# Optimization experiments

Hardware: AMD Instinct MI355X
Metric: run time of the kernel (lower is better)

## Reference

```python
import jax, jax.numpy as jnp
import numpy as np

B, S, H, NH, NF = 128, 1024, 768, 8, 8
FUSED = 3 * H + NF  # 2312


def _lin(k, o, i):
    return jax.random.normal(k, (o, i), jnp.float32) * (1.0 / np.sqrt(i))


def setup_inputs() -> dict:
    key = jax.random.key(0)
    ks = jax.random.split(key, 20)
    last_hidden = jax.random.normal(ks[0], (B, S, H), jnp.float32)
    arousal_feats = jax.random.normal(ks[1], (B, NF), jnp.float32)
    sep1 = jax.random.randint(ks[2], (B,), 2, 800)
    sep2 = jnp.minimum(sep1 + jax.random.randint(ks[3], (B,), 2, 200), S - 1)
    return {
        "last_hidden": last_hidden,
        "arousal_feats": arousal_feats,
        "sep1": sep1,
        "sep2": sep2,
        "in_proj_w": _lin(ks[4], 3 * H, H),
        "in_proj_b": jnp.zeros((3 * H,), jnp.float32),
        "out_w": _lin(ks[5], H, H),
        "out_b": jnp.zeros((H,), jnp.float32),
        "ln_g": jnp.ones((NF,), jnp.float32),
        "ln_b": jnp.zeros((NF,), jnp.float32),
        "va_w1": _lin(ks[6], 512, FUSED),
        "va_b1": jnp.zeros((512,), jnp.float32),
        "va_w2": _lin(ks[7], 128, 512),
        "va_b2": jnp.zeros((128,), jnp.float32),
        "va_w3": _lin(ks[8], 2, 128),
        "va_b3": jnp.zeros((2,), jnp.float32),
        "pol_w": _lin(ks[9], 3, FUSED),
        "pol_b": jnp.zeros((3,), jnp.float32),
        "aro_w": _lin(ks[10], 3, FUSED),
        "aro_b": jnp.zeros((3,), jnp.float32),
    }


def reference(last_hidden, arousal_feats, sep1, sep2, in_proj_w, in_proj_b,
              out_w, out_b, ln_g, ln_b, va_w1, va_b1, va_w2, va_b2,
              va_w3, va_b3, pol_w, pol_b, aro_w, aro_b):
    b, s, h = last_hidden.shape
    nh, dh = NH, h // NH
    pos = jnp.arange(s)[None, :]  # [1,S]
    # ragged boundaries -> masks (honors s1>1 / s2>s1+1 fallbacks to CLS token)
    text_mask = jnp.where((sep1 > 1)[:, None], (pos >= 1) & (pos < sep1[:, None]), pos == 0)
    asp_mask = jnp.where((sep2 > sep1 + 1)[:, None], (pos > sep1[:, None]) & (pos < sep2[:, None]), pos == 0)
    amf = asp_mask.astype(last_hidden.dtype)
    asp_query = (last_hidden * amf[..., None]).sum(1) / amf.sum(1)[:, None]  # [B,H]
    # MultiheadAttention with a single query per sample, keys/values masked to text span
    wq, wk, wv = jnp.split(in_proj_w, 3, axis=0)
    bq, bk, bv = jnp.split(in_proj_b, 3)
    q = (asp_query @ wq.T + bq).reshape(b, nh, dh)
    k = (last_hidden @ wk.T + bk).reshape(b, s, nh, dh)
    v = (last_hidden @ wv.T + bv).reshape(b, s, nh, dh)
    scale = 1.0 / np.sqrt(dh)
    scores = jnp.einsum('bhd,bshd->bhs', q, k) * scale
    scores = jnp.where(text_mask[:, None, :], scores, -jnp.inf)
    attn = jax.nn.softmax(scores, axis=-1)
    ctx = jnp.einsum('bhs,bshd->bhd', attn, v).reshape(b, h)
    cross = ctx @ out_w.T + out_b  # [B,H]
    # ArousalFeatureNorm ~ LayerNorm over feature dim
    mu = arousal_feats.mean(-1, keepdims=True)
    var = arousal_feats.var(-1, keepdims=True)
    aro_n = (arousal_feats - mu) / jnp.sqrt(var + 1e-5) * ln_g + ln_b
    fused = jnp.concatenate([last_hidden[:, 0], cross, asp_query, aro_n], axis=-1)
    hdn = jax.nn.gelu(fused @ va_w1.T + va_b1, approximate=False)
    hdn = jax.nn.gelu(hdn @ va_w2.T + va_b2, approximate=False)
    va = hdn @ va_w3.T + va_b3
    pol = fused @ pol_w.T + pol_b
    aro = fused @ aro_w.T + aro_b
    return (va, pol, aro)
```

## Files before the change

### kernel.cpp

```cpp
#include <hip/hip_runtime.h>
#include <hip/hip_bf16.h>
#include <math.h>

#define B 128
#define S 1024
#define H 768
#define NH 8
#define DH 96
#define FUSED 2312
#define FPAD 2432
#define KSPLIT 19
#define KCHUNK 128
#define ASL 8
#define NSL 8
#define FCH 16
#define SCALE 0.10206207261596575f
#define GELU_C 0.70710678118654752f

__device__ __forceinline__ float dot4(float4 a, float4 b) {
    return a.x * b.x + a.y * b.y + a.z * b.z + a.w * b.w;
}

__global__ void aspq_part_kernel(const float* __restrict__ lh,
                                 const int* __restrict__ sep1,
                                 const int* __restrict__ sep2,
                                 float* __restrict__ aspp) {
    int b = blockIdx.x, z = blockIdx.y, t = threadIdx.x;
    int s1 = sep1[b], s2 = sep2[b];
    int lo, hi;
    if (s2 > s1 + 1) { lo = s1 + 1; hi = s2; } else { lo = 0; hi = 1; }
    const float* base = lh + ((size_t)b * S) * H + 4 * t;
    float4 a = {0.f, 0.f, 0.f, 0.f};
    for (int s = lo + z; s < hi; s += ASL) {
        float4 r = *(const float4*)(base + (size_t)s * H);
        a.x += r.x; a.y += r.y; a.z += r.z; a.w += r.w;
    }
    *(float4*)(aspp + (size_t)z * (B * H) + b * H + 4 * t) = a;
}

__global__ void qu_kernel(const float* __restrict__ aspp,
                          const int* __restrict__ sep1,
                          const int* __restrict__ sep2,
                          const float* __restrict__ wq,
                          const float* __restrict__ bq,
                          const float* __restrict__ wk,
                          float* __restrict__ aspq,
                          float* __restrict__ U) {
    int b = blockIdx.x, h = blockIdx.y, t = threadIdx.x;
    int s1 = sep1[b], s2 = sep2[b];
    int lo, hi;
    if (s2 > s1 + 1) { lo = s1 + 1; hi = s2; } else { lo = 0; hi = 1; }
    float inv = 1.0f / (float)(hi - lo);
    __shared__ float aq[H];
    __shared__ float qh[DH];
    for (int c = t; c < H; c += 256) {
        float a = 0.f;
#pragma unroll
        for (int z = 0; z < ASL; ++z)
            a += aspp[(size_t)z * (B * H) + b * H + c];
        a *= inv;
        aq[c] = a;
        if (h == 0) aspq[b * H + c] = a;
    }
    __syncthreads();
    int wave = t >> 6, lane = t & 63;
#pragma unroll
    for (int i = 0; i < 24; ++i) {
        int d = wave * 24 + i;
        const float* wrow = wq + (size_t)(h * DH + d) * H;
        float a = 0.f;
#pragma unroll
        for (int j = 0; j < H / 64; ++j) a += wrow[lane + 64 * j] * aq[lane + 64 * j];
        for (int off = 32; off; off >>= 1) a += __shfl_xor(a, off);
        if (lane == 0) qh[d] = a + bq[h * DH + d];
    }
    __syncthreads();
    float u0 = 0.f, u1 = 0.f, u2 = 0.f;
    for (int d = 0; d < DH; ++d) {
        const float* wrow = wk + (size_t)(h * DH + d) * H;
        float qd = qh[d];
        u0 += qd * wrow[t];
        u1 += qd * wrow[t + 256];
        u2 += qd * wrow[t + 512];
    }
    float* Ub = U + ((size_t)b * NH + h) * H;
    Ub[t] = u0; Ub[t + 256] = u1; Ub[t + 512] = u2;
}

__global__ __launch_bounds__(512) void flash_kernel(
        const float* __restrict__ lhg,
        const float* __restrict__ U,
        const int* __restrict__ sep1,
        float* __restrict__ Op,
        float* __restrict__ mlb) {
    int b = blockIdx.x, z = blockIdx.y, t = threadIdx.x;
    int wave = t >> 6, lane = t & 63;
    int s1 = sep1[b];
    int tlo = (s1 > 1) ? 1 : 0;
    int thi = (s1 > 1) ? s1 : 1;
    int span = thi - tlo;
    int nrows = (span > z) ? ((span - z - 1) / NSL + 1) : 0;

    __shared__ float lhs[FCH][H];

    const float4* Uh = (const float4*)(U + ((size_t)b * NH + wave) * H);
    float4 u0 = Uh[lane], u1 = Uh[lane + 64], u2 = Uh[lane + 128];
    float4 O0 = {0.f, 0.f, 0.f, 0.f}, O1 = O0, O2 = O0;
    float m = -1e30f, l = 0.f;

    int rid = t >> 5;
    int cid = t & 31;

    for (int j0 = 0; j0 < nrows; j0 += FCH) {
        int nv = min(FCH, nrows - j0);
        if (rid < nv) {
            int sg = tlo + z + NSL * (j0 + rid);
            const float4* row = (const float4*)(lhg + ((size_t)b * S + sg) * H);
            float4* dst = (float4*)lhs[rid];
#pragma unroll
            for (int k = 0; k < 6; ++k) dst[cid + 32 * k] = row[cid + 32 * k];
        }
        __syncthreads();
        for (int r = 0; r < nv; ++r) {
            const float4* xr = (const float4*)lhs[r];
            float4 x0 = xr[lane], x1 = xr[lane + 64], x2 = xr[lane + 128];
            float s = dot4(u0, x0) + dot4(u1, x1) + dot4(u2, x2);
            for (int off = 32; off; off >>= 1) s += __shfl_xor(s, off);
            s *= SCALE;
            if (s <= m) {
                float p = __expf(s - m);
                l += p;
                O0.x += p * x0.x; O0.y += p * x0.y; O0.z += p * x0.z; O0.w += p * x0.w;
                O1.x += p * x1.x; O1.y += p * x1.y; O1.z += p * x1.z; O1.w += p * x1.w;
                O2.x += p * x2.x; O2.y += p * x2.y; O2.z += p * x2.z; O2.w += p * x2.w;
            } else {
                float c = __expf(m - s);
                m = s;
                l = l * c + 1.0f;
                O0.x = O0.x * c + x0.x; O0.y = O0.y * c + x0.y;
                O0.z = O0.z * c + x0.z; O0.w = O0.w * c + x0.w;
                O1.x = O1.x * c + x1.x; O1.y = O1.y * c + x1.y;
                O1.z = O1.z * c + x1.z; O1.w = O1.w * c + x1.w;
                O2.x = O2.x * c + x2.x; O2.y = O2.y * c + x2.y;
                O2.z = O2.z * c + x2.z; O2.w = O2.w * c + x2.w;
            }
        }
        __syncthreads();
    }
    float4* Ob = (float4*)(Op + (((size_t)z * B + b) * NH + wave) * H);
    Ob[lane] = O0; Ob[lane + 64] = O1; Ob[lane + 128] = O2;
    if (lane == 0) {
        float* ml = mlb + ((size_t)z * B + b) * NH * 2;
        ml[2 * wave]     = m;
        ml[2 * wave + 1] = l;
    }
}

__global__ void mergectx_kernel(const float* __restrict__ Op,
                                const float* __restrict__ mlb,
                                const float* __restrict__ wv,
                                const float* __restrict__ bv,
                                float* __restrict__ ctx) {
    int b = blockIdx.x, h = blockIdx.y, t = threadIdx.x;
    float M = -1e30f;
#pragma unroll
    for (int z = 0; z < NSL; ++z)
        M = fmaxf(M, mlb[(((size_t)z * B + b) * NH + h) * 2]);
    float wz[NSL], L = 0.f;
#pragma unroll
    for (int z = 0; z < NSL; ++z) {
        const float* ml = mlb + (((size_t)z * B + b) * NH + h) * 2;
        float e = __expf(ml[0] - M);
        wz[z] = e;
        L += e * ml[1];
    }
    float Li = 1.0f / L;
    __shared__ float wsum[H];
    for (int c = t; c < H; c += 256) {
        float a = 0.f;
#pragma unroll
        for (int z = 0; z < NSL; ++z)
            a += wz[z] * Op[(((size_t)z * B + b) * NH + h) * H + c];
        wsum[c] = a * Li;
    }
    __syncthreads();
    int wave = t >> 6, lane = t & 63;
#pragma unroll
    for (int i = 0; i < 24; ++i) {
        int d = wave * 24 + i;
        const float* wrow = wv + (size_t)(h * DH + d) * H;
        float a = 0.f;
#pragma unroll
        for (int j = 0; j < H / 64; ++j) a += wrow[lane + 64 * j] * wsum[lane + 64 * j];
        for (int off = 32; off; off >>= 1) a += __shfl_xor(a, off);
        if (lane == 0) ctx[b * H + h * DH + d] = a + bv[h * DH + d];
    }
}

template <int TAG, bool KCL>
__global__ void gemm_kernel(const float* __restrict__ A, int lda, int a_bs,
                            const float* __restrict__ W, int ldw, int w_bs,
                            float* __restrict__ C, int ldc, int c_bs,
                            int M, int N, int K, int kclamp) {
    A += (size_t)blockIdx.z * a_bs;
    W += (size_t)blockIdx.z * w_bs;
    C += (size_t)blockIdx.z * c_bs;
    int kcl = KCL ? (kclamp - (int)blockIdx.z * w_bs) : 0;
    int n0 = blockIdx.x * 32, m0 = blockIdx.y * 32;
    __shared__ float As[32][33];
    __shared__ float Ws[32][33];
    int t = threadIdx.x;
    int tx = t & 31, ty = t >> 5;
    int lr = t >> 3, lc = (t & 7) * 4;
    float acc[4] = {0.f, 0.f, 0.f, 0.f};
    for (int k0 = 0; k0 < K; k0 += 32) {
        {
            float4 a = *(const float4*)(A + (size_t)(m0 + lr) * lda + k0 + lc);
            As[lr][lc] = a.x; As[lr][lc + 1] = a.y;
            As[lr][lc + 2] = a.z; As[lr][lc + 3] = a.w;
        }
        {
            int kk = k0 + lc;
            if (KCL) kk = min(kk, kcl);
            float4 w = *(const float4*)(W + (size_t)(n0 + lr) * ldw + kk);
            Ws[lr][lc] = w.x; Ws[lr][lc + 1] = w.y;
            Ws[lr][lc + 2] = w.z; Ws[lr][lc + 3] = w.w;
        }
        __syncthreads();
#pragma unroll
        for (int kk = 0; kk < 32; ++kk) {
            float wv = Ws[tx][kk];
#pragma unroll
            for (int i = 0; i < 4; ++i)
                acc[i] += As[ty + 8 * i][kk] * wv;
        }
        __syncthreads();
    }
    int n = n0 + tx;
#pragma unroll
    for (int i = 0; i < 4; ++i) {
        int m = m0 + ty + 8 * i;
        C[(size_t)m * ldc + n] = acc[i];
    }
}

__global__ void fuse_kernel(const float* __restrict__ lh,
                            const float* __restrict__ crossp,
                            const float* __restrict__ out_b,
                            const float* __restrict__ aspq,
                            const float* __restrict__ aro_f,
                            const float* __restrict__ ln_g,
                            const float* __restrict__ ln_b,
                            float* __restrict__ fused) {
    int b = blockIdx.x, t = threadIdx.x;
    float* fb = fused + (size_t)b * FPAD;
    const float* lhb = lh + (size_t)b * S * H;
    for (int i = t; i < H; i += 256) {
        float cr = out_b[i];
#pragma unroll
        for (int z = 0; z < 6; ++z) cr += crossp[(size_t)z * (B * H) + b * H + i];
        fb[i]         = lhb[i];
        fb[H + i]     = cr;
        fb[2 * H + i] = aspq[b * H + i];
    }
    for (int i = t; i < FPAD - FUSED; i += 256) fb[FUSED + i] = 0.f;
    if (t < 8) {
        const float* af = aro_f + b * 8;
        float mu = 0.f;
#pragma unroll
        for (int j = 0; j < 8; ++j) mu += af[j];
        mu *= 0.125f;
        float var = 0.f;
#pragma unroll
        for (int j = 0; j < 8; ++j) { float d = af[j] - mu; var += d * d; }
        var *= 0.125f;
        fb[3 * H + t] = (af[t] - mu) * rsqrtf(var + 1e-5f) * ln_g[t] + ln_b[t];
    }
}

__global__ void mlp2_kernel(const float* __restrict__ hdn1p,
                            const float* __restrict__ fusedb,
                            const float* __restrict__ va_b1,
                            const float* __restrict__ va_w2,
                            const float* __restrict__ va_b2,
                            const float* __restrict__ va_w3,
                            const float* __restrict__ va_b3,
                            const float* __restrict__ pol_w,
                            const float* __restrict__ pol_b,
                            const float* __restrict__ aro_w,
                            const float* __restrict__ aro_b,
                            float* __restrict__ out) {
    int b = blockIdx.x, t = threadIdx.x;
    __shared__ float hs[512];
    __shared__ float h2[128];
    for (int n = t; n < 512; n += 256) {
        float sacc = 0.f;
#pragma unroll
        for (int z = 0; z < KSPLIT; ++z)
            sacc += hdn1p[(size_t)z * (B * 512) + b * 512 + n];
        sacc += va_b1[n];
        hs[n] = 0.5f * sacc * (1.0f + erff(sacc * GELU_C));
    }
    __syncthreads();
    int wave = t >> 6, lane = t & 63;
    for (int i = 0; i < 32; ++i) {
        int n = wave * 32 + i;
        float a = 0.f;
#pragma unroll
        for (int j = 0; j < 8; ++j) {
            int k = lane + 64 * j;
            a += hs[k] * va_w2[(size_t)n * 512 + k];
        }
        for (int off = 32; off; off >>= 1) a += __shfl_xor(a, off);
        if (lane == 0) {
            float x = a + va_b2[n];
            h2[n] = 0.5f * x * (1.0f + erff(x * GELU_C));
        }
    }
    __syncthreads();
    const float* fb = fusedb + (size_t)b * FPAD;
    for (int oi = 0; oi < 2; ++oi) {
        int o = wave * 2 + oi;
        float acc = 0.f, bia;
        float* dst;
        if (o < 2) {
            for (int k = lane; k < 128; k += 64) acc += h2[k] * va_w3[o * 128 + k];
            bia = va_b3[o]; dst = out + b * 2 + o;
        } else if (o < 5) {
            int r = o - 2;
            for (int k = lane; k < FUSED; k += 64) acc += fb[k] * pol_w[(size_t)r * FUSED + k];
            bia = pol_b[r]; dst = out + 256 + b * 3 + r;
        } else {
            int r = o - 5;
            for (int k = lane; k < FUSED; k += 64) acc += fb[k] * aro_w[(size_t)r * FUSED + k];
            bia = aro_b[r]; dst = out + 640 + b * 3 + r;
        }
        for (int off = 32; off; off >>= 1) acc += __shfl_xor(acc, off);
        if (lane == 0) *dst = acc + bia;
    }
}

extern "C" void kernel_launch(void* const* d_in, const int* in_sizes, int n_in,
                              void* d_out, int out_size, void* d_ws, size_t ws_size,
                              hipStream_t stream) {
    const float* lh    = (const float*)d_in[0];
    const float* aro_f = (const float*)d_in[1];
    const int*   sep1  = (const int*)d_in[2];
    const int*   sep2  = (const int*)d_in[3];
    const float* in_w  = (const float*)d_in[4];
    const float* in_b  = (const float*)d_in[5];
    const float* out_w = (const float*)d_in[6];
    const float* out_b = (const float*)d_in[7];
    const float* ln_g  = (const float*)d_in[8];
    const float* ln_b  = (const float*)d_in[9];
    const float* va_w1 = (const float*)d_in[10];
    const float* va_b1 = (const float*)d_in[11];
    const float* va_w2 = (const float*)d_in[12];
    const float* va_b2 = (const float*)d_in[13];
    const float* va_w3 = (const float*)d_in[14];
    const float* va_b3 = (const float*)d_in[15];
    const float* pol_w = (const float*)d_in[16];
    const float* pol_b = (const float*)d_in[17];
    const float* aro_w = (const float*)d_in[18];
    const float* aro_b = (const float*)d_in[19];
    float* out = (float*)d_out;

    float* ws = (float*)d_ws;
    float* aspp   = ws;
    float* aspq   = aspp + ASL * B * H;
    float* Ubuf   = aspq + B * H;
    float* Opb    = Ubuf + B * NH * H;
    float* mlbuf  = Opb + (size_t)NSL * B * NH * H;
    float* ctx    = mlbuf + NSL * B * NH * 2;
    float* crossp = ctx + B * H;
    float* fusedb = crossp + 6 * B * H;
    float* hdn1p  = fusedb + B * FPAD;

    const float* wq = in_w;
    const float* wk = in_w + H * H;
    const float* wv = in_w + 2 * H * H;
    const float* bq = in_b;
    const float* bv = in_b + 2 * H;

    aspq_part_kernel<<<dim3(B, ASL), 192, 0, stream>>>(lh, sep1, sep2, aspp);
    qu_kernel<<<dim3(B, NH), 256, 0, stream>>>(aspp, sep1, sep2, wq, bq, wk,
                                               aspq, Ubuf);
    flash_kernel<<<dim3(B, NSL), 512, 0, stream>>>(lh, Ubuf, sep1, Opb, mlbuf);
    mergectx_kernel<<<dim3(B, NH), 256, 0, stream>>>(Opb, mlbuf, wv, bv, ctx);
    gemm_kernel<3, false><<<dim3(24, 4, 6), 256, 0, stream>>>(
        ctx, H, KCHUNK, out_w, H, KCHUNK, crossp, H, B * H, B, H, KCHUNK, 0);
    fuse_kernel<<<B, 256, 0, stream>>>(lh, crossp, out_b, aspq, aro_f,
                                       ln_g, ln_b, fusedb);
    gemm_kernel<4, true><<<dim3(16, 4, KSPLIT), 256, 0, stream>>>(
        fusedb, FPAD, KCHUNK, va_w1, FUSED, KCHUNK,
        hdn1p, 512, B * 512, B, 512, KCHUNK, FUSED - 4);
    mlp2_kernel<<<B, 256, 0, stream>>>(hdn1p, fusedb, va_b1, va_w2, va_b2,
                                       va_w3, va_b3, pol_w, pol_b,
                                       aro_w, aro_b, out);
}
```

Before: 244.9 us.

## Fuse context merge, output projection, fused-vector build and heads per sample

Replaces the merge-ctx, split-K output projection GEMM and fuse kernels with one per-sample kernel. It merges the flash partials, projects through wv and out_w with wave-level matvecs, builds the fused vector in shared memory and computes the pol/aro heads there. mlp2 is slimmed and moved to 512 threads. This removes launches and intermediate global buffers, but only 128 blocks now stream both full weight matrices, which reduces parallelism.

```diff
diff --git a/kernel.cpp b/kernel.cpp
--- a/kernel.cpp
+++ b/kernel.cpp
@@ -19,6 +19,10 @@
 
 __device__ __forceinline__ float dot4(float4 a, float4 b) {
     return a.x * b.x + a.y * b.y + a.z * b.z + a.w * b.w;
+}
+
+__device__ __forceinline__ float gelu(float x) {
+    return 0.5f * x * (1.0f + erff(x * GELU_C));
 }
 
 __global__ void aspq_part_kernel(const float* __restrict__ lh,
@@ -156,44 +160,122 @@
     }
 }
 
-__global__ void mergectx_kernel(const float* __restrict__ Op,
-                                const float* __restrict__ mlb,
-                                const float* __restrict__ wv,
-                                const float* __restrict__ bv,
-                                float* __restrict__ ctx) {
-    int b = blockIdx.x, h = blockIdx.y, t = threadIdx.x;
-    float M = -1e30f;
-#pragma unroll
-    for (int z = 0; z < NSL; ++z)
-        M = fmaxf(M, mlb[(((size_t)z * B + b) * NH + h) * 2]);
-    float wz[NSL], L = 0.f;
-#pragma unroll
-    for (int z = 0; z < NSL; ++z) {
-        const float* ml = mlb + (((size_t)z * B + b) * NH + h) * 2;
-        float e = __expf(ml[0] - M);
-        wz[z] = e;
-        L += e * ml[1];
-    }
-    float Li = 1.0f / L;
-    __shared__ float wsum[H];
-    for (int c = t; c < H; c += 256) {
+__global__ __launch_bounds__(512) void mergefuse_kernel(
+        const float* __restrict__ Op,
+        const float* __restrict__ mlb,
+        const float* __restrict__ wv,
+        const float* __restrict__ bv,
+        const float* __restrict__ out_w,
+        const float* __restrict__ out_b,
+        const float* __restrict__ lh,
+        const float* __restrict__ aspq,
+        const float* __restrict__ aro_f,
+        const float* __restrict__ ln_g,
+        const float* __restrict__ ln_b,
+        const float* __restrict__ pol_w,
+        const float* __restrict__ pol_b,
+        const float* __restrict__ aro_w,
+        const float* __restrict__ aro_b,
+        float* __restrict__ fused,
+        float* __restrict__ out) {
+    int b = blockIdx.x, t = threadIdx.x;
+    int wave = t >> 6, lane = t & 63;
+    __shared__ float wsumS[NH * H];
+    __shared__ float ctxS[H];
+    __shared__ float fusedS[FPAD];
+
+    const float* lhb = lh + (size_t)b * S * H;
+    for (int i = t; i < H; i += 512) {
+        fusedS[i]          = lhb[i];
+        fusedS[2 * H + i]  = aspq[b * H + i];
+    }
+    for (int i = FUSED + t; i < FPAD; i += 512) fusedS[i] = 0.f;
+    if (t < 8) {
+        const float* af = aro_f + b * 8;
+        float mu = 0.f;
+#pragma unroll
+        for (int j = 0; j < 8; ++j) mu += af[j];
+        mu *= 0.125f;
+        float var = 0.f;
+#pragma unroll
+        for (int j = 0; j < 8; ++j) { float d = af[j] - mu; var += d * d; }
+        var *= 0.125f;
+        fusedS[3 * H + t] = (af[t] - mu) * rsqrtf(var + 1e-5f) * ln_g[t] + ln_b[t];
+    }
+
+    {
+        int h = wave;
+        float M = -1e30f;
+#pragma unroll
+        for (int z = 0; z < NSL; ++z)
+            M = fmaxf(M, mlb[(((size_t)z * B + b) * NH + h) * 2]);
+        float wzv[NSL], L = 0.f;
+#pragma unroll
+        for (int z = 0; z < NSL; ++z) {
+            const float* ml = mlb + (((size_t)z * B + b) * NH + h) * 2;
+            float e = __expf(ml[0] - M);
+            wzv[z] = e;
+            L += e * ml[1];
+        }
+        float Li = 1.0f / L;
+        for (int c = lane; c < H; c += 64) {
+            float a = 0.f;
+#pragma unroll
+            for (int z = 0; z < NSL; ++z)
+                a += wzv[z] * Op[(((size_t)z * B + b) * NH + h) * H + c];
+            wsumS[h * H + c] = a * Li;
+        }
+    }
+    __syncthreads();
+
+    {
+        const float4* ws4 = (const float4*)(wsumS + wave * H);
+        float4 s0 = ws4[lane], s1 = ws4[lane + 64], s2 = ws4[lane + 128];
+        for (int i = 0; i < 96; ++i) {
+            int o = wave * 96 + i;
+            const float4* wr = (const float4*)(wv + (size_t)o * H);
+            float a = dot4(wr[lane], s0) + dot4(wr[lane + 64], s1)
+                    + dot4(wr[lane + 128], s2);
+            for (int off = 32; off; off >>= 1) a += __shfl_xor(a, off);
+            if (lane == 0) ctxS[o] = a + bv[o];
+        }
+    }
+    __syncthreads();
+
+    {
+        const float4* c4 = (const float4*)ctxS;
+        float4 s0 = c4[lane], s1 = c4[lane + 64], s2 = c4[lane + 128];
+        for (int i = 0; i < 96; ++i) {
+            int o = wave * 96 + i;
+            const float4* wr = (const float4*)(out_w + (size_t)o * H);
+            float a = dot4(wr[lane], s0) + dot4(wr[lane + 64], s1)
+                    + dot4(wr[lane + 128], s2);
+            for (int off = 32; off; off >>= 1) a += __shfl_xor(a, off);
+            if (lane == 0) fusedS[H + o] = a + out_b[o];
+        }
+    }
+    __syncthreads();
+
+    {
+        const float4* fs4 = (const float4*)fusedS;
+        float4* fg4 = (float4*)(fused + (size_t)b * FPAD);
+        for (int i = t; i < FPAD / 4; i += 512) fg4[i] = fs4[i];
+    }
+    if (wave < 6) {
+        int r = (wave < 3) ? wave : wave - 3;
+        const float* w = (wave < 3) ? (pol_w + (size_t)r * FUSED)
+                                    : (aro_w + (size_t)r * FUSED);
         float a = 0.f;
 #pragma unroll
-        for (int z = 0; z < NSL; ++z)
-            a += wz[z] * Op[(((size_t)z * B + b) * NH + h) * H + c];
-        wsum[c] = a * Li;
-    }
-    __syncthreads();
-    int wave = t >> 6, lane = t & 63;
-#pragma unroll
-    for (int i = 0; i < 24; ++i) {
-        int d = wave * 24 + i;
-        const float* wrow = wv + (size_t)(h * DH + d) * H;
-        float a = 0.f;
-#pragma unroll
-        for (int j = 0; j < H / 64; ++j) a += wrow[lane + 64 * j] * wsum[lane + 64 * j];
+        for (int j = 0; j < 37; ++j) {
+            int k = lane + 64 * j;
+            if (k < FUSED) a += fusedS[k] * w[k];
+        }
         for (int off = 32; off; off >>= 1) a += __shfl_xor(a, off);
-        if (lane == 0) ctx[b * H + h * DH + d] = a + bv[h * DH + d];
+        if (lane == 0) {
+            if (wave < 3) out[256 + b * 3 + r] = a + pol_b[r];
+            else          out[640 + b * 3 + r] = a + aro_b[r];
+        }
     }
 }
 
@@ -244,99 +326,44 @@
     }
 }
 
-__global__ void fuse_kernel(const float* __restrict__ lh,
-                            const float* __restrict__ crossp,
-                            const float* __restrict__ out_b,
-                            const float* __restrict__ aspq,
-                            const float* __restrict__ aro_f,
-                            const float* __restrict__ ln_g,
-                            const float* __restrict__ ln_b,
-                            float* __restrict__ fused) {
+__global__ __launch_bounds__(512) void mlp2_kernel(
+        const float* __restrict__ hdn1p,
+        const float* __restrict__ va_b1,
+        const float* __restrict__ va_w2,
+        const float* __restrict__ va_b2,
+        const float* __restrict__ va_w3,
+        const float* __restrict__ va_b3,
+        float* __restrict__ out) {
     int b = blockIdx.x, t = threadIdx.x;
-    float* fb = fused + (size_t)b * FPAD;
-    const float* lhb = lh + (size_t)b * S * H;
-    for (int i = t; i < H; i += 256) {
-        float cr = out_b[i];
-#pragma unroll
-        for (int z = 0; z < 6; ++z) cr += crossp[(size_t)z * (B * H) + b * H + i];
-        fb[i]         = lhb[i];
-        fb[H + i]     = cr;
-        fb[2 * H + i] = aspq[b * H + i];
-    }
-    for (int i = t; i < FPAD - FUSED; i += 256) fb[FUSED + i] = 0.f;
-    if (t < 8) {
-        const float* af = aro_f + b * 8;
-        float mu = 0.f;
-#pragma unroll
-        for (int j = 0; j < 8; ++j) mu += af[j];
-        mu *= 0.125f;
-        float var = 0.f;
-#pragma unroll
-        for (int j = 0; j < 8; ++j) { float d = af[j] - mu; var += d * d; }
-        var *= 0.125f;
-        fb[3 * H + t] = (af[t] - mu) * rsqrtf(var + 1e-5f) * ln_g[t] + ln_b[t];
-    }
-}
-
-__global__ void mlp2_kernel(const float* __restrict__ hdn1p,
-                            const float* __restrict__ fusedb,
-                            const float* __restrict__ va_b1,
-                            const float* __restrict__ va_w2,
-                            const float* __restrict__ va_b2,
-                            const float* __restrict__ va_w3,
-                            const float* __restrict__ va_b3,
-                            const float* __restrict__ pol_w,
-                            const float* __restrict__ pol_b,
-                            const float* __restrict__ aro_w,
-                            const float* __restrict__ aro_b,
-                            float* __restrict__ out) {
-    int b = blockIdx.x, t = threadIdx.x;
-    __shared__ float hs[512];
-    __shared__ float h2[128];
-    for (int n = t; n < 512; n += 256) {
-        float sacc = 0.f;
+    int wave = t >> 6, lane = t & 63;
+    __shared__ float hsS[512];
+    __shared__ float h2S[128];
+    {
+        float s = 0.f;
 #pragma unroll
         for (int z = 0; z < KSPLIT; ++z)
-            sacc += hdn1p[(size_t)z * (B * 512) + b * 512 + n];
-        sacc += va_b1[n];
-        hs[n] = 0.5f * sacc * (1.0f + erff(sacc * GELU_C));
-    }
-    __syncthreads();
-    int wave = t >> 6, lane = t & 63;
-    for (int i = 0; i < 32; ++i) {
-        int n = wave * 32 + i;
+            s += hdn1p[(size_t)z * (B * 512) + b * 512 + t];
+        hsS[t] = gelu(s + va_b1[t]);
+    }
+    __syncthreads();
+#pragma unroll
+    for (int i = 0; i < 16; ++i) {
+        int n = wave * 16 + i;
         float a = 0.f;
 #pragma unroll
         for (int j = 0; j < 8; ++j) {
             int k = lane + 64 * j;
-            a += hs[k] * va_w2[(size_t)n * 512 + k];
+            a += hsS[k] * va_w2[(size_t)n * 512 + k];
         }
         for (int off = 32; off; off >>= 1) a += __shfl_xor(a, off);
-        if (lane == 0) {
-            float x = a + va_b2[n];
-            h2[n] = 0.5f * x * (1.0f + erff(x * GELU_C));
-        }
-    }
-    __syncthreads();
-    const float* fb = fusedb + (size_t)b * FPAD;
-    for (int oi = 0; oi < 2; ++oi) {
-        int o = wave * 2 + oi;
-        float acc = 0.f, bia;
-        float* dst;
-        if (o < 2) {
-            for (int k = lane; k < 128; k += 64) acc += h2[k] * va_w3[o * 128 + k];
-            bia = va_b3[o]; dst = out + b * 2 + o;
-        } else if (o < 5) {
-            int r = o - 2;
-            for (int k = lane; k < FUSED; k += 64) acc += fb[k] * pol_w[(size_t)r * FUSED + k];
-            bia = pol_b[r]; dst = out + 256 + b * 3 + r;
-        } else {
-            int r = o - 5;
-            for (int k = lane; k < FUSED; k += 64) acc += fb[k] * aro_w[(size_t)r * FUSED + k];
-            bia = aro_b[r]; dst = out + 640 + b * 3 + r;
-        }
-        for (int off = 32; off; off >>= 1) acc += __shfl_xor(acc, off);
-        if (lane == 0) *dst = acc + bia;
+        if (lane == 0) h2S[n] = gelu(a + va_b2[n]);
+    }
+    __syncthreads();
+    if (wave < 2) {
+        float a = h2S[lane] * va_w3[wave * 128 + lane]
+                + h2S[lane + 64] * va_w3[wave * 128 + lane + 64];
+        for (int off = 32; off; off >>= 1) a += __shfl_xor(a, off);
+        if (lane == 0) out[b * 2 + wave] = a + va_b3[wave];
     }
 }
 
@@ -371,9 +398,7 @@
     float* Ubuf   = aspq + B * H;
     float* Opb    = Ubuf + B * NH * H;
     float* mlbuf  = Opb + (size_t)NSL * B * NH * H;
-    float* ctx    = mlbuf + NSL * B * NH * 2;
-    float* crossp = ctx + B * H;
-    float* fusedb = crossp + 6 * B * H;
+    float* fusedb = mlbuf + NSL * B * NH * 2;
     float* hdn1p  = fusedb + B * FPAD;
 
     const float* wq = in_w;
@@ -386,15 +411,13 @@
     qu_kernel<<<dim3(B, NH), 256, 0, stream>>>(aspp, sep1, sep2, wq, bq, wk,
                                                aspq, Ubuf);
     flash_kernel<<<dim3(B, NSL), 512, 0, stream>>>(lh, Ubuf, sep1, Opb, mlbuf);
-    mergectx_kernel<<<dim3(B, NH), 256, 0, stream>>>(Opb, mlbuf, wv, bv, ctx);
-    gemm_kernel<3, false><<<dim3(24, 4, 6), 256, 0, stream>>>(
-        ctx, H, KCHUNK, out_w, H, KCHUNK, crossp, H, B * H, B, H, KCHUNK, 0);
-    fuse_kernel<<<B, 256, 0, stream>>>(lh, crossp, out_b, aspq, aro_f,
-                                       ln_g, ln_b, fusedb);
+    mergefuse_kernel<<<B, 512, 0, stream>>>(Opb, mlbuf, wv, bv, out_w, out_b,
+                                            lh, aspq, aro_f, ln_g, ln_b,
+                                            pol_w, pol_b, aro_w, aro_b,
+                                            fusedb, out);
     gemm_kernel<4, true><<<dim3(16, 4, KSPLIT), 256, 0, stream>>>(
         fusedb, FPAD, KCHUNK, va_w1, FUSED, KCHUNK,
         hdn1p, 512, B * 512, B, 512, KCHUNK, FUSED - 4);
-    mlp2_kernel<<<B, 256, 0, stream>>>(hdn1p, fusedb, va_b1, va_w2, va_b2,
-                                       va_w3, va_b3, pol_w, pol_b,
-                                       aro_w, aro_b, out);
-}
+    mlp2_kernel<<<B, 512, 0, stream>>>(hdn1p, va_b1, va_w2, va_b2,
+                                       va_w3, va_b3, out);
+}
```

Result: slower. 307.9 us (+25.7%).

## Batch eight samples per block in qu and mergectx kernels to reuse weight tiles

Applied to the files above, without the earlier changes.

The q/U projection and the context merge kernels now each process eight batch samples per block. Weight tiles (wq, wk, wv) are staged through shared memory and reused across the eight samples, instead of every (sample, head) block streaming the full per-head weight slice from global memory. This cuts weight traffic by about eight times. The cost is a grid with eight times fewer blocks (128 instead of 1024), more shared memory per block, and extra syncthreads.

```diff
diff --git a/kernel.cpp b/kernel.cpp
--- a/kernel.cpp
+++ b/kernel.cpp
@@ -14,6 +14,7 @@
 #define ASL 8
 #define NSL 8
 #define FCH 16
+#define NB 8
 #define SCALE 0.10206207261596575f
 #define GELU_C 0.70710678118654752f
 
@@ -38,53 +39,84 @@
     *(float4*)(aspp + (size_t)z * (B * H) + b * H + 4 * t) = a;
 }
 
-__global__ void qu_kernel(const float* __restrict__ aspp,
-                          const int* __restrict__ sep1,
-                          const int* __restrict__ sep2,
-                          const float* __restrict__ wq,
-                          const float* __restrict__ bq,
-                          const float* __restrict__ wk,
-                          float* __restrict__ aspq,
-                          float* __restrict__ U) {
-    int b = blockIdx.x, h = blockIdx.y, t = threadIdx.x;
-    int s1 = sep1[b], s2 = sep2[b];
-    int lo, hi;
-    if (s2 > s1 + 1) { lo = s1 + 1; hi = s2; } else { lo = 0; hi = 1; }
-    float inv = 1.0f / (float)(hi - lo);
-    __shared__ float aq[H];
-    __shared__ float qh[DH];
-    for (int c = t; c < H; c += 256) {
+__global__ __launch_bounds__(256) void qu_kernel(
+        const float* __restrict__ aspp,
+        const int* __restrict__ sep1,
+        const int* __restrict__ sep2,
+        const float* __restrict__ wq,
+        const float* __restrict__ bq,
+        const float* __restrict__ wk,
+        float* __restrict__ aspq,
+        float* __restrict__ U) {
+    int g = blockIdx.x, h = blockIdx.y, t = threadIdx.x;
+    int b0 = g * NB;
+    __shared__ float aq[NB][772];
+    __shared__ float Wt[96][33];
+    __shared__ float qS[NB][100];
+    __shared__ float WkS[96][68];
+
+    for (int i = t; i < NB * H; i += 256) {
+        int b = i / H, c = i - b * H;
+        int gb = b0 + b;
+        int s1 = sep1[gb], s2 = sep2[gb];
+        int n = (s2 > s1 + 1) ? (s2 - s1 - 1) : 1;
         float a = 0.f;
 #pragma unroll
         for (int z = 0; z < ASL; ++z)
-            a += aspp[(size_t)z * (B * H) + b * H + c];
-        a *= inv;
-        aq[c] = a;
-        if (h == 0) aspq[b * H + c] = a;
-    }
-    __syncthreads();
-    int wave = t >> 6, lane = t & 63;
-#pragma unroll
-    for (int i = 0; i < 24; ++i) {
-        int d = wave * 24 + i;
-        const float* wrow = wq + (size_t)(h * DH + d) * H;
-        float a = 0.f;
-#pragma unroll
-        for (int j = 0; j < H / 64; ++j) a += wrow[lane + 64 * j] * aq[lane + 64 * j];
-        for (int off = 32; off; off >>= 1) a += __shfl_xor(a, off);
-        if (lane == 0) qh[d] = a + bq[h * DH + d];
-    }
-    __syncthreads();
-    float u0 = 0.f, u1 = 0.f, u2 = 0.f;
-    for (int d = 0; d < DH; ++d) {
-        const float* wrow = wk + (size_t)(h * DH + d) * H;
-        float qd = qh[d];
-        u0 += qd * wrow[t];
-        u1 += qd * wrow[t + 256];
-        u2 += qd * wrow[t + 512];
-    }
-    float* Ub = U + ((size_t)b * NH + h) * H;
-    Ub[t] = u0; Ub[t + 256] = u1; Ub[t + 512] = u2;
+            a += aspp[(size_t)z * (B * H) + (size_t)gb * H + c];
+        a /= (float)n;
+        aq[b][c] = a;
+        if (h == 0) aspq[(size_t)gb * H + c] = a;
+    }
+    __syncthreads();
+
+    int tb = t & 7, tn = t >> 3;
+    float qacc[3] = {0.f, 0.f, 0.f};
+    for (int k0 = 0; k0 < H; k0 += 32) {
+#pragma unroll
+        for (int j = 0; j < 3; ++j) {
+            int e4 = t + 256 * j;
+            int r = e4 >> 3, c4 = (e4 & 7) * 4;
+            float4 w = *(const float4*)(wq + (size_t)(h * DH + r) * H + k0 + c4);
+            Wt[r][c4] = w.x; Wt[r][c4 + 1] = w.y;
+            Wt[r][c4 + 2] = w.z; Wt[r][c4 + 3] = w.w;
+        }
+        __syncthreads();
+#pragma unroll
+        for (int kk = 0; kk < 32; ++kk) {
+            float av = aq[tb][k0 + kk];
+#pragma unroll
+            for (int j = 0; j < 3; ++j)
+                qacc[j] += av * Wt[tn + 32 * j][kk];
+        }
+        __syncthreads();
+    }
+#pragma unroll
+    for (int j = 0; j < 3; ++j)
+        qS[tb][tn + 32 * j] = qacc[j] + bq[h * DH + tn + 32 * j];
+    __syncthreads();
+
+    for (int c0 = 0; c0 < H; c0 += 64) {
+#pragma unroll
+        for (int j = 0; j < 6; ++j) {
+            int e4 = t + 256 * j;
+            int r = e4 >> 4, c4 = (e4 & 15) * 4;
+            float4 w = *(const float4*)(wk + (size_t)(h * DH + r) * H + c0 + c4);
+            WkS[r][c4] = w.x; WkS[r][c4 + 1] = w.y;
+            WkS[r][c4 + 2] = w.z; WkS[r][c4 + 3] = w.w;
+        }
+        __syncthreads();
+#pragma unroll
+        for (int jj = 0; jj < 2; ++jj) {
+            int cl = tn + 32 * jj;
+            float a = 0.f;
+#pragma unroll
+            for (int d = 0; d < 96; ++d)
+                a += qS[tb][d] * WkS[d][cl];
+            U[((size_t)(b0 + tb) * NH + h) * H + c0 + cl] = a;
+        }
+        __syncthreads();
+    }
 }
 
 __global__ __launch_bounds__(512) void flash_kernel(
@@ -156,44 +188,71 @@
     }
 }
 
-__global__ void mergectx_kernel(const float* __restrict__ Op,
-                                const float* __restrict__ mlb,
-                                const float* __restrict__ wv,
-                                const float* __restrict__ bv,
-                                float* __restrict__ ctx) {
-    int b = blockIdx.x, h = blockIdx.y, t = threadIdx.x;
-    float M = -1e30f;
-#pragma unroll
-    for (int z = 0; z < NSL; ++z)
-        M = fmaxf(M, mlb[(((size_t)z * B + b) * NH + h) * 2]);
-    float wz[NSL], L = 0.f;
-#pragma unroll
-    for (int z = 0; z < NSL; ++z) {
-        const float* ml = mlb + (((size_t)z * B + b) * NH + h) * 2;
-        float e = __expf(ml[0] - M);
-        wz[z] = e;
-        L += e * ml[1];
-    }
-    float Li = 1.0f / L;
-    __shared__ float wsum[H];
-    for (int c = t; c < H; c += 256) {
+__global__ __launch_bounds__(256) void mergectx_kernel(
+        const float* __restrict__ Op,
+        const float* __restrict__ mlb,
+        const float* __restrict__ wv,
+        const float* __restrict__ bv,
+        float* __restrict__ ctx) {
+    int g = blockIdx.x, h = blockIdx.y, t = threadIdx.x;
+    int b0 = g * NB;
+    __shared__ float wsum[NB][772];
+    __shared__ float Wt[96][33];
+    __shared__ float wzS[NB][NSL];
+    __shared__ float LiS[NB];
+
+    if (t < NB) {
+        int gb = b0 + t;
+        float M = -1e30f;
+#pragma unroll
+        for (int z = 0; z < NSL; ++z)
+            M = fmaxf(M, mlb[(((size_t)z * B + gb) * NH + h) * 2]);
+        float L = 0.f;
+#pragma unroll
+        for (int z = 0; z < NSL; ++z) {
+            const float* ml = mlb + (((size_t)z * B + gb) * NH + h) * 2;
+            float e = __expf(ml[0] - M);
+            wzS[t][z] = e;
+            L += e * ml[1];
+        }
+        LiS[t] = 1.0f / L;
+    }
+    __syncthreads();
+    for (int i = t; i < NB * H; i += 256) {
+        int b = i / H, c = i - b * H;
         float a = 0.f;
 #pragma unroll
         for (int z = 0; z < NSL; ++z)
-            a += wz[z] * Op[(((size_t)z * B + b) * NH + h) * H + c];
-        wsum[c] = a * Li;
-    }
-    __syncthreads();
-    int wave = t >> 6, lane = t & 63;
-#pragma unroll
-    for (int i = 0; i < 24; ++i) {
-        int d = wave * 24 + i;
-        const float* wrow = wv + (size_t)(h * DH + d) * H;
-        float a = 0.f;
-#pragma unroll
-        for (int j = 0; j < H / 64; ++j) a += wrow[lane + 64 * j] * wsum[lane + 64 * j];
-        for (int off = 32; off; off >>= 1) a += __shfl_xor(a, off);
-        if (lane == 0) ctx[b * H + h * DH + d] = a + bv[h * DH + d];
+            a += wzS[b][z] * Op[(((size_t)z * B + b0 + b) * NH + h) * H + c];
+        wsum[b][c] = a * LiS[b];
+    }
+    __syncthreads();
+
+    int tb = t & 7, tn = t >> 3;
+    float acc[3] = {0.f, 0.f, 0.f};
+    for (int k0 = 0; k0 < H; k0 += 32) {
+#pragma unroll
+        for (int j = 0; j < 3; ++j) {
+            int e4 = t + 256 * j;
+            int r = e4 >> 3, c4 = (e4 & 7) * 4;
+            float4 w = *(const float4*)(wv + (size_t)(h * DH + r) * H + k0 + c4);
+            Wt[r][c4] = w.x; Wt[r][c4 + 1] = w.y;
+            Wt[r][c4 + 2] = w.z; Wt[r][c4 + 3] = w.w;
+        }
+        __syncthreads();
+#pragma unroll
+        for (int kk = 0; kk < 32; ++kk) {
+            float av = wsum[tb][k0 + kk];
+#pragma unroll
+            for (int j = 0; j < 3; ++j)
+                acc[j] += av * Wt[tn + 32 * j][kk];
+        }
+        __syncthreads();
+    }
+#pragma unroll
+    for (int j = 0; j < 3; ++j) {
+        int d = tn + 32 * j;
+        ctx[(size_t)(b0 + tb) * H + h * DH + d] = acc[j] + bv[h * DH + d];
     }
 }
 
@@ -383,10 +442,10 @@
     const float* bv = in_b + 2 * H;
 
     aspq_part_kernel<<<dim3(B, ASL), 192, 0, stream>>>(lh, sep1, sep2, aspp);
-    qu_kernel<<<dim3(B, NH), 256, 0, stream>>>(aspp, sep1, sep2, wq, bq, wk,
-                                               aspq, Ubuf);
+    qu_kernel<<<dim3(B / NB, NH), 256, 0, stream>>>(aspp, sep1, sep2, wq, bq,
+                                                    wk, aspq, Ubuf);
     flash_kernel<<<dim3(B, NSL), 512, 0, stream>>>(lh, Ubuf, sep1, Opb, mlbuf);
-    mergectx_kernel<<<dim3(B, NH), 256, 0, stream>>>(Opb, mlbuf, wv, bv, ctx);
+    mergectx_kernel<<<dim3(B / NB, NH), 256, 0, stream>>>(Opb, mlbuf, wv, bv, ctx);
     gemm_kernel<3, false><<<dim3(24, 4, 6), 256, 0, stream>>>(
         ctx, H, KCHUNK, out_w, H, KCHUNK, crossp, H, B * H, B, H, KCHUNK, 0);
     fuse_kernel<<<B, 256, 0, stream>>>(lh, crossp, out_b, aspq, aro_f,
```

After: 316.8 us. +29.3%, slower.
